# Kernel optimization log

Measured on AMD Instinct MI355X. Metric: run time of the kernel, lower is better.

The kernel has to match this reference:

```python
import jax, jax.numpy as jnp
import numpy as np

BN_EPS = 1e-5


def setup_inputs() -> dict:
    key = jax.random.key(0)
    k1, k2 = jax.random.split(key, 2)
    b, C, h, w = 4, 256, 64, 64
    K = 16  # num_codes is hard-coded to 16 inside __init__
    x = jax.random.normal(k1, (b, C, h, w), dtype=jnp.float32)
    conv_w = jax.random.normal(k2, (K, C), dtype=jnp.float32) * (1.0 / np.sqrt(C))
    bn_gamma = jnp.ones((K,), dtype=jnp.float32)
    bn_beta = jnp.zeros((K,), dtype=jnp.float32)
    return {"x": x, "conv_w": conv_w, "bn_gamma": bn_gamma, "bn_beta": bn_beta}


def reference(x, conv_w, bn_gamma, bn_beta):
    b, C, h, w = x.shape
    K = conv_w.shape[0]
    hw = h * w

    # 1x1 conv (no bias) -> BatchNorm2d (training-mode batch stats) -> ReLU
    cw = jnp.einsum('kc,bchw->bkhw', conv_w, x)          # (b, K, h, w)
    mean = cw.mean(axis=(0, 2, 3))                        # (K,)
    var = cw.var(axis=(0, 2, 3))                          # biased variance, (K,)
    cw = (cw - mean[None, :, None, None]) * jax.lax.rsqrt(var + BN_EPS)[None, :, None, None]
    cw = cw * bn_gamma[None, :, None, None] + bn_beta[None, :, None, None]
    cw = jax.nn.relu(cw)

    cw_flat = cw.reshape(b, K, hw)                        # (b, K, hw)
    scale = cw_flat.mean(axis=2)                          # (b, K)
    # Faithful to torch: flat row-major reinterpretation of (b,K,hw) as (b,hw,K,1)
    r = cw_flat.reshape(b, hw, K, 1)                      # (b, hw, K, 1)

    x2 = x.reshape(b, C, hw).transpose(0, 2, 1)           # (b, hw, C)
    diff = x2[:, :, None, :] - r                          # (b, hw, K, C)

    scaled_l2 = scale[:, :, None] * jnp.sum(diff * diff, axis=1)   # (b, K, C)
    aw = jax.nn.softmax(scaled_l2, axis=1)                # softmax over K, (b, K, C)
    encoded_feat = jnp.sum(aw[:, None, :, :] * diff, axis=1)       # (b, K, C)
    return encoded_feat
```

## Files before the change

kernel.cpp:

```cpp
#include <hip/hip_runtime.h>

#define BN_EPS 1e-5f

#define OFF_PBN     0
#define OFF_PSR     8192
#define OFF_PSX     24576
#define OFF_PSXX    155648
#define OFF_CROSSR  286720
#define OFF_CW      352256
#define OFF_PCX     614400
#define WS_NEED     ((size_t)(OFF_PCX + 2097152) * sizeof(float))

#define CONV_FMA(W, K0)                                  \
    acc[K0][0] = fmaf(W, xv.x, acc[K0][0]);              \
    acc[K0][1] = fmaf(W, xv.y, acc[K0][1]);              \
    acc[K0][2] = fmaf(W, xv.z, acc[K0][2]);              \
    acc[K0][3] = fmaf(W, xv.w, acc[K0][3]);

#define FMA16(v, rp)                                     \
    {                                                    \
        const float4* rq_ = (const float4*)(rp);         \
        float4 r0_ = rq_[0], r1_ = rq_[1];               \
        float4 r2_ = rq_[2], r3_ = rq_[3];               \
        acc[0]  = fmaf(v, r0_.x, acc[0]);                \
        acc[1]  = fmaf(v, r0_.y, acc[1]);                \
        acc[2]  = fmaf(v, r0_.z, acc[2]);                \
        acc[3]  = fmaf(v, r0_.w, acc[3]);                \
        acc[4]  = fmaf(v, r1_.x, acc[4]);                \
        acc[5]  = fmaf(v, r1_.y, acc[5]);                \
        acc[6]  = fmaf(v, r1_.z, acc[6]);                \
        acc[7]  = fmaf(v, r1_.w, acc[7]);                \
        acc[8]  = fmaf(v, r2_.x, acc[8]);                \
        acc[9]  = fmaf(v, r2_.y, acc[9]);                \
        acc[10] = fmaf(v, r2_.z, acc[10]);               \
        acc[11] = fmaf(v, r2_.w, acc[11]);               \
        acc[12] = fmaf(v, r3_.x, acc[12]);               \
        acc[13] = fmaf(v, r3_.y, acc[13]);               \
        acc[14] = fmaf(v, r3_.z, acc[14]);               \
        acc[15] = fmaf(v, r3_.w, acc[15]);               \
    }

__global__ __launch_bounds__(256, 2) void k_conv(const float* __restrict__ x,
                                                 const float* __restrict__ w,
                                                 float* __restrict__ cw,
                                                 float* __restrict__ pbn) {
    __shared__ float wlT[4124];
    __shared__ float bnl[4][32];
    int bid = blockIdx.x;
    int b   = bid >> 6;
    int ich = bid & 63;
    int t   = threadIdx.x;
    int cp  = t & 15;
    int il  = t >> 4;
    int wv  = t >> 6;

    for (int m = t; m < 4096; m += 256) {
        int k = m >> 8, c = m & 255;
        wlT[(c << 4) + ((c >> 5) << 2) + k] = w[m];
    }
    __syncthreads();

    float acc[16][4];
    #pragma unroll
    for (int k = 0; k < 16; ++k) {
        #pragma unroll
        for (int e = 0; e < 4; ++e) acc[k][e] = 0.f;
    }

    const float* xp = x + (size_t)(b * 256 + cp * 16) * 4096 + ich * 64 + il * 4;
    #pragma unroll
    for (int cc = 0; cc < 16; ++cc) {
        float4 xv = *(const float4*)(xp + (size_t)cc * 4096);
        int c = cp * 16 + cc;
        const float4* wr = (const float4*)&wlT[(c << 4) + ((c >> 5) << 2)];
        float4 w0 = wr[0], w1 = wr[1], w2 = wr[2], w3 = wr[3];
        CONV_FMA(w0.x, 0)  CONV_FMA(w0.y, 1)  CONV_FMA(w0.z, 2)  CONV_FMA(w0.w, 3)
        CONV_FMA(w1.x, 4)  CONV_FMA(w1.y, 5)  CONV_FMA(w1.z, 6)  CONV_FMA(w1.w, 7)
        CONV_FMA(w2.x, 8)  CONV_FMA(w2.y, 9)  CONV_FMA(w2.z, 10) CONV_FMA(w2.w, 11)
        CONV_FMA(w3.x, 12) CONV_FMA(w3.y, 13) CONV_FMA(w3.z, 14) CONV_FMA(w3.w, 15)
    }

    float r8[8][4];
    #pragma unroll
    for (int r = 0; r < 8; ++r) {
        #pragma unroll
        for (int e = 0; e < 4; ++e) {
            float lo = acc[r][e]     + __shfl_xor(acc[r][e], 1);
            float hi = acc[r + 8][e] + __shfl_xor(acc[r + 8][e], 1);
            r8[r][e] = (cp & 1) ? hi : lo;
        }
    }
    float r4v[4][4];
    #pragma unroll
    for (int r = 0; r < 4; ++r) {
        #pragma unroll
        for (int e = 0; e < 4; ++e) {
            float lo = r8[r][e]     + __shfl_xor(r8[r][e], 2);
            float hi = r8[r + 4][e] + __shfl_xor(r8[r + 4][e], 2);
            r4v[r][e] = (cp & 2) ? hi : lo;
        }
    }
    float r2[2][4];
    #pragma unroll
    for (int r = 0; r < 2; ++r) {
        #pragma unroll
        for (int e = 0; e < 4; ++e) {
            float lo = r4v[r][e]     + __shfl_xor(r4v[r][e], 4);
            float hi = r4v[r + 2][e] + __shfl_xor(r4v[r + 2][e], 4);
            r2[r][e] = (cp & 4) ? hi : lo;
        }
    }
    float r1[4];
    #pragma unroll
    for (int e = 0; e < 4; ++e) {
        float lo = r2[0][e] + __shfl_xor(r2[0][e], 8);
        float hi = r2[1][e] + __shfl_xor(r2[1][e], 8);
        r1[e] = (cp & 8) ? hi : lo;
    }
    int ko = ((cp & 1) << 3) | (((cp >> 1) & 1) << 2) | (((cp >> 2) & 1) << 1)
           | ((cp >> 3) & 1);

    float4 st;
    st.x = r1[0]; st.y = r1[1]; st.z = r1[2]; st.w = r1[3];
    *(float4*)(cw + (size_t)b * 65536 + (size_t)ko * 4096 + ich * 64 + il * 4) = st;

    float s1 = r1[0] + r1[1] + r1[2] + r1[3];
    float s2 = r1[0]*r1[0] + r1[1]*r1[1] + r1[2]*r1[2] + r1[3]*r1[3];
    #pragma unroll
    for (int m = 16; m <= 32; m <<= 1) {
        s1 += __shfl_xor(s1, m);
        s2 += __shfl_xor(s2, m);
    }
    if ((t & 48) == 0) { bnl[wv][ko] = s1; bnl[wv][16 + ko] = s2; }
    __syncthreads();
    if (t < 32) {
        pbn[bid * 32 + t] = bnl[0][t] + bnl[1][t] + bnl[2][t] + bnl[3][t];
    }
}

template <bool PCX>
__global__ __launch_bounds__(256, 2) void k_main(const float* __restrict__ x,
                                                 const float* __restrict__ gamma,
                                                 const float* __restrict__ beta,
                                                 float* __restrict__ ws,
                                                 float* __restrict__ pcx) {
    __shared__ float xl[8192];
    __shared__ float rl[512];
    __shared__ float red1[256], red2[256];
    __shared__ float bnred[256];
    int bid = blockIdx.x;
    int b   = bid >> 7;
    int s   = bid & 127;
    int kp  = s >> 3;
    int t   = threadIdx.x;

    {
        int col = t & 31, row0 = t >> 5;
        float p = 0.f;
        for (int m = row0; m < 256; m += 8) p += ws[OFF_PBN + m * 32 + col];
        bnred[t] = p;
    }
    __syncthreads();
    float s1 = 0.f, s2 = 0.f;
    #pragma unroll
    for (int j = 0; j < 8; ++j) {
        s1 += bnred[j * 32 + kp];
        s2 += bnred[j * 32 + 16 + kp];
    }
    float mean = s1 * (1.f / 16384.f);
    float var  = s2 * (1.f / 16384.f) - mean * mean;
    float aa   = gamma[kp] * rsqrtf(var + BN_EPS);
    float bb   = beta[kp] - mean * aa;

    #pragma unroll
    for (int j = 0; j < 8; ++j) {
        int F  = j * 256 + t;
        int cc = F >> 3, i4 = F & 7;
        const float* pa = x + (size_t)(b * 256 + cc) * 4096 + s * 32 + i4 * 4;
        float4 v = *(const float4*)pa;
        int ib = i4 * 4;
        xl[(ib + 0) * 256 + (cc ^ (ib + 0))] = v.x;
        xl[(ib + 1) * 256 + (cc ^ (ib + 1))] = v.y;
        xl[(ib + 2) * 256 + (cc ^ (ib + 2))] = v.z;
        xl[(ib + 3) * 256 + (cc ^ (ib + 3))] = v.w;
    }

    const float* cwp = ws + OFF_CW + (size_t)b * 65536 + (size_t)kp * 4096
                     + (size_t)(s & 7) * 512;
    float sr = 0.f, srr = 0.f;
    #pragma unroll
    for (int j = 0; j < 2; ++j) {
        float v = cwp[t + j * 256];
        v = fmaxf(fmaf(v, aa, bb), 0.f);
        rl[t + j * 256] = v;
        sr += v; srr += v * v;
    }
    red1[t] = sr; red2[t] = srr;
    __syncthreads();

    if (t < 16) {
        float a1 = 0.f, a2 = 0.f;
        for (int m = t; m < 256; m += 16) { a1 += red1[m]; a2 += red2[m]; }
        ws[OFF_PSR + bid * 32 + t]      = a1;
        ws[OFF_PSR + bid * 32 + 16 + t] = a2;
    }

    int c = t;
    float acc[16];
    #pragma unroll
    for (int k = 0; k < 16; ++k) acc[k] = 0.f;
    float xs = 0.f, xs2 = 0.f;
    #pragma unroll
    for (int ii = 0; ii < 32; ++ii) {
        float xv = xl[ii * 256 + (c ^ ii)];
        xs += xv; xs2 += xv * xv;
        FMA16(xv, rl + ii * 16);
    }

    ws[OFF_PSX  + bid * 256 + c] = xs;
    ws[OFF_PSXX + bid * 256 + c] = xs2;
    if (PCX) {
        float* pp = pcx + (size_t)(bid * 16) * 256 + c;
        #pragma unroll
        for (int k = 0; k < 16; ++k) pp[(size_t)k * 256] = acc[k];
    } else {
        #pragma unroll
        for (int k = 0; k < 16; ++k)
            atomicAdd(ws + OFF_CROSSR + (b * 16 + k) * 256 + c, acc[k]);
    }
}

__global__ __launch_bounds__(256) void k_red(const float* __restrict__ pcx,
                                             float* __restrict__ crossr) {
    int bid = blockIdx.x;
    int b  = bid >> 6;
    int k  = (bid >> 2) & 15;
    int sg = bid & 3;
    int c  = threadIdx.x;
    float acc = 0.f;
    #pragma unroll 8
    for (int m = 0; m < 32; ++m) {
        int sl = sg * 32 + m;
        acc += pcx[(size_t)((b * 128 + sl) * 16 + k) * 256 + c];
    }
    crossr[((sg * 4 + b) * 16 + k) * 256 + c] = acc;
}

__global__ __launch_bounds__(256) void k_final(const float* __restrict__ ws,
                                               float* __restrict__ out) {
    __shared__ float srl[4096];
    __shared__ float fin[48];
    int b = blockIdx.x;
    int t = threadIdx.x;

    const float* psr = ws + OFF_PSR + (size_t)b * 128 * 32;
    #pragma unroll
    for (int j = 0; j < 16; ++j) srl[j * 256 + t] = psr[j * 256 + t];
    __syncthreads();

    if (t < 16) {
        float v = 0.f;
        for (int s = 0; s < 128; ++s) v += srl[s * 32 + t];
        fin[t] = v;
    } else if (t < 32) {
        int k = t - 16;
        float v = 0.f;
        for (int s = 0; s < 128; ++s) v += srl[s * 32 + 16 + k];
        fin[16 + k] = v;
    } else if (t < 48) {
        int kp = t - 32;
        float v = 0.f;
        for (int s = kp * 8; s < kp * 8 + 8; ++s)
            for (int k2 = 0; k2 < 16; ++k2) v += srl[s * 32 + k2];
        fin[32 + kp] = v;
    }
    __syncthreads();

    int c = t;
    float sx = 0.f, sxx = 0.f;
    const float* psx  = ws + OFF_PSX  + (size_t)b * 128 * 256;
    const float* psxx = ws + OFF_PSXX + (size_t)b * 128 * 256;
    for (int p = 0; p < 128; ++p) {
        sx  += psx[p * 256 + c];
        sxx += psxx[p * 256 + c];
    }

    float sl2[16];
    float mx = -1e30f;
    #pragma unroll
    for (int k = 0; k < 16; ++k) {
        float cr = 0.f;
        #pragma unroll
        for (int sg = 0; sg < 4; ++sg)
            cr += ws[OFF_CROSSR + ((sg * 4 + b) * 16 + k) * 256 + c];
        float v = fin[32 + k] * (1.f / 4096.f) * (sxx - 2.f * cr + fin[16 + k]);
        sl2[k] = v;
        mx = fmaxf(mx, v);
    }
    float den = 0.f;
    #pragma unroll
    for (int k = 0; k < 16; ++k) {
        float e = __expf(sl2[k] - mx);
        sl2[k] = e;
        den += e;
    }
    float inv = 1.f / den;
    #pragma unroll
    for (int k = 0; k < 16; ++k)
        out[(size_t)(b * 16 + k) * 256 + c] = sl2[k] * inv * (sx - fin[k]);
}

extern "C" void kernel_launch(void* const* d_in, const int* in_sizes, int n_in,
                              void* d_out, int out_size, void* d_ws, size_t ws_size,
                              hipStream_t stream) {
    const float* x     = (const float*)d_in[0];
    const float* w     = (const float*)d_in[1];
    const float* gamma = (const float*)d_in[2];
    const float* beta  = (const float*)d_in[3];
    float* ws  = (float*)d_ws;
    float* out = (float*)d_out;

    bool use_pcx = ws_size >= WS_NEED;

    k_conv<<<256, 256, 0, stream>>>(x, w, ws + OFF_CW, ws + OFF_PBN);
    if (use_pcx) {
        k_main<true><<<512, 256, 0, stream>>>(x, gamma, beta, ws, ws + OFF_PCX);
        k_red<<<256, 256, 0, stream>>>(ws + OFF_PCX, ws + OFF_CROSSR);
    } else {
        hipMemsetAsync(ws + OFF_CROSSR, 0, 65536 * sizeof(float), stream);
        k_main<false><<<512, 256, 0, stream>>>(x, gamma, beta, ws, nullptr);
    }
    k_final<<<4, 256, 0, stream>>>(ws, out);
}
```

Before: 102.3 us.

## Restructure conv kernel to stage x tile in LDS across 512 blocks

```diff
diff --git a/kernel.cpp b/kernel.cpp
--- a/kernel.cpp
+++ b/kernel.cpp
@@ -3,19 +3,13 @@
 #define BN_EPS 1e-5f
 
 #define OFF_PBN     0
-#define OFF_PSR     8192
-#define OFF_PSX     24576
-#define OFF_PSXX    155648
-#define OFF_CROSSR  286720
-#define OFF_CW      352256
-#define OFF_PCX     614400
+#define OFF_PSR     16384
+#define OFF_PSX     32768
+#define OFF_PSXX    163840
+#define OFF_CROSSR  294912
+#define OFF_CW      360448
+#define OFF_PCX     622592
 #define WS_NEED     ((size_t)(OFF_PCX + 2097152) * sizeof(float))
-
-#define CONV_FMA(W, K0)                                  \
-    acc[K0][0] = fmaf(W, xv.x, acc[K0][0]);              \
-    acc[K0][1] = fmaf(W, xv.y, acc[K0][1]);              \
-    acc[K0][2] = fmaf(W, xv.z, acc[K0][2]);              \
-    acc[K0][3] = fmaf(W, xv.w, acc[K0][3]);
 
 #define FMA16(v, rp)                                     \
     {                                                    \
@@ -41,104 +35,75 @@
     }
 
 __global__ __launch_bounds__(256, 2) void k_conv(const float* __restrict__ x,
-                                                 const float* __restrict__ w,
+                                                 const float* __restrict__ wq,
                                                  float* __restrict__ cw,
                                                  float* __restrict__ pbn) {
+    __shared__ float xl[10240];
     __shared__ float wlT[4124];
-    __shared__ float bnl[4][32];
+    __shared__ float comb[512];
+    __shared__ float bnr1[128], bnr2[128];
     int bid = blockIdx.x;
-    int b   = bid >> 6;
-    int ich = bid & 63;
+    int b   = bid >> 7;
+    int s   = bid & 127;
     int t   = threadIdx.x;
-    int cp  = t & 15;
-    int il  = t >> 4;
-    int wv  = t >> 6;
+    int k   = t & 15;
+    int q   = t >> 4;
+    int iq  = q & 7;
+    int h   = q >> 3;
 
     for (int m = t; m < 4096; m += 256) {
-        int k = m >> 8, c = m & 255;
-        wlT[(c << 4) + ((c >> 5) << 2) + k] = w[m];
-    }
-    __syncthreads();
-
-    float acc[16][4];
-    #pragma unroll
-    for (int k = 0; k < 16; ++k) {
+        int kk = m >> 8, c = m & 255;
+        wlT[(c << 4) + ((c >> 5) << 2) + kk] = wq[m];
+    }
+    #pragma unroll
+    for (int j = 0; j < 8; ++j) {
+        int F  = j * 256 + t;
+        int cc = F >> 3, i4 = F & 7;
+        float4 v = *(const float4*)(x + (size_t)(b * 256 + cc) * 4096
+                                    + s * 32 + i4 * 4);
+        xl[cc * 40 + i4 * 4 + 0] = v.x;
+        xl[cc * 40 + i4 * 4 + 1] = v.y;
+        xl[cc * 40 + i4 * 4 + 2] = v.z;
+        xl[cc * 40 + i4 * 4 + 3] = v.w;
+    }
+    __syncthreads();
+
+    float a0 = 0.f, a1 = 0.f, a2 = 0.f, a3 = 0.f;
+    int c0 = h * 128;
+    #pragma unroll 8
+    for (int cc = 0; cc < 128; ++cc) {
+        int c = c0 + cc;
+        float4 xv = *(const float4*)&xl[c * 40 + iq * 4];
+        float wv  = wlT[(c << 4) + ((c >> 5) << 2) + k];
+        a0 = fmaf(wv, xv.x, a0);
+        a1 = fmaf(wv, xv.y, a1);
+        a2 = fmaf(wv, xv.z, a2);
+        a3 = fmaf(wv, xv.w, a3);
+    }
+    if (h == 1) {
+        int p = t & 127;
+        comb[p * 4 + 0] = a0; comb[p * 4 + 1] = a1;
+        comb[p * 4 + 2] = a2; comb[p * 4 + 3] = a3;
+    }
+    __syncthreads();
+    if (h == 0) {
+        a0 += comb[t * 4 + 0]; a1 += comb[t * 4 + 1];
+        a2 += comb[t * 4 + 2]; a3 += comb[t * 4 + 3];
+        float4 o; o.x = a0; o.y = a1; o.z = a2; o.w = a3;
+        *(float4*)(cw + (size_t)b * 65536 + (size_t)k * 4096 + s * 32 + iq * 4) = o;
+        bnr1[iq * 16 + k] = a0 + a1 + a2 + a3;
+        bnr2[iq * 16 + k] = a0 * a0 + a1 * a1 + a2 * a2 + a3 * a3;
+    }
+    __syncthreads();
+    if (t < 16) {
+        float s1 = 0.f, s2 = 0.f;
         #pragma unroll
-        for (int e = 0; e < 4; ++e) acc[k][e] = 0.f;
-    }
-
-    const float* xp = x + (size_t)(b * 256 + cp * 16) * 4096 + ich * 64 + il * 4;
-    #pragma unroll
-    for (int cc = 0; cc < 16; ++cc) {
-        float4 xv = *(const float4*)(xp + (size_t)cc * 4096);
-        int c = cp * 16 + cc;
-        const float4* wr = (const float4*)&wlT[(c << 4) + ((c >> 5) << 2)];
-        float4 w0 = wr[0], w1 = wr[1], w2 = wr[2], w3 = wr[3];
-        CONV_FMA(w0.x, 0)  CONV_FMA(w0.y, 1)  CONV_FMA(w0.z, 2)  CONV_FMA(w0.w, 3)
-        CONV_FMA(w1.x, 4)  CONV_FMA(w1.y, 5)  CONV_FMA(w1.z, 6)  CONV_FMA(w1.w, 7)
-        CONV_FMA(w2.x, 8)  CONV_FMA(w2.y, 9)  CONV_FMA(w2.z, 10) CONV_FMA(w2.w, 11)
-        CONV_FMA(w3.x, 12) CONV_FMA(w3.y, 13) CONV_FMA(w3.z, 14) CONV_FMA(w3.w, 15)
-    }
-
-    float r8[8][4];
-    #pragma unroll
-    for (int r = 0; r < 8; ++r) {
-        #pragma unroll
-        for (int e = 0; e < 4; ++e) {
-            float lo = acc[r][e]     + __shfl_xor(acc[r][e], 1);
-            float hi = acc[r + 8][e] + __shfl_xor(acc[r + 8][e], 1);
-            r8[r][e] = (cp & 1) ? hi : lo;
-        }
-    }
-    float r4v[4][4];
-    #pragma unroll
-    for (int r = 0; r < 4; ++r) {
-        #pragma unroll
-        for (int e = 0; e < 4; ++e) {
-            float lo = r8[r][e]     + __shfl_xor(r8[r][e], 2);
-            float hi = r8[r + 4][e] + __shfl_xor(r8[r + 4][e], 2);
-            r4v[r][e] = (cp & 2) ? hi : lo;
-        }
-    }
-    float r2[2][4];
-    #pragma unroll
-    for (int r = 0; r < 2; ++r) {
-        #pragma unroll
-        for (int e = 0; e < 4; ++e) {
-            float lo = r4v[r][e]     + __shfl_xor(r4v[r][e], 4);
-            float hi = r4v[r + 2][e] + __shfl_xor(r4v[r + 2][e], 4);
-            r2[r][e] = (cp & 4) ? hi : lo;
-        }
-    }
-    float r1[4];
-    #pragma unroll
-    for (int e = 0; e < 4; ++e) {
-        float lo = r2[0][e] + __shfl_xor(r2[0][e], 8);
-        float hi = r2[1][e] + __shfl_xor(r2[1][e], 8);
-        r1[e] = (cp & 8) ? hi : lo;
-    }
-    int ko = ((cp & 1) << 3) | (((cp >> 1) & 1) << 2) | (((cp >> 2) & 1) << 1)
-           | ((cp >> 3) & 1);
-
-    float4 st;
-    st.x = r1[0]; st.y = r1[1]; st.z = r1[2]; st.w = r1[3];
-    *(float4*)(cw + (size_t)b * 65536 + (size_t)ko * 4096 + ich * 64 + il * 4) = st;
-
-    float s1 = r1[0] + r1[1] + r1[2] + r1[3];
-    float s2 = r1[0]*r1[0] + r1[1]*r1[1] + r1[2]*r1[2] + r1[3]*r1[3];
-    #pragma unroll
-    for (int m = 16; m <= 32; m <<= 1) {
-        s1 += __shfl_xor(s1, m);
-        s2 += __shfl_xor(s2, m);
-    }
-    if ((t & 48) == 0) { bnl[wv][ko] = s1; bnl[wv][16 + ko] = s2; }
-    __syncthreads();
-    if (t < 32) {
-        pbn[bid * 32 + t] = bnl[0][t] + bnl[1][t] + bnl[2][t] + bnl[3][t];
-    }
-}
-
-template <bool PCX>
+        for (int j = 0; j < 8; ++j) { s1 += bnr1[j * 16 + t]; s2 += bnr2[j * 16 + t]; }
+        pbn[bid * 32 + t]      = s1;
+        pbn[bid * 32 + 16 + t] = s2;
+    }
+}
+
 __global__ __launch_bounds__(256, 2) void k_main(const float* __restrict__ x,
                                                  const float* __restrict__ gamma,
                                                  const float* __restrict__ beta,
@@ -157,7 +122,7 @@
     {
         int col = t & 31, row0 = t >> 5;
         float p = 0.f;
-        for (int m = row0; m < 256; m += 8) p += ws[OFF_PBN + m * 32 + col];
+        for (int m = row0; m < 512; m += 8) p += ws[OFF_PBN + m * 32 + col];
         bnred[t] = p;
     }
     __syncthreads();
@@ -219,15 +184,9 @@
 
     ws[OFF_PSX  + bid * 256 + c] = xs;
     ws[OFF_PSXX + bid * 256 + c] = xs2;
-    if (PCX) {
-        float* pp = pcx + (size_t)(bid * 16) * 256 + c;
-        #pragma unroll
-        for (int k = 0; k < 16; ++k) pp[(size_t)k * 256] = acc[k];
-    } else {
-        #pragma unroll
-        for (int k = 0; k < 16; ++k)
-            atomicAdd(ws + OFF_CROSSR + (b * 16 + k) * 256 + c, acc[k]);
-    }
+    float* pp = pcx + (size_t)(bid * 16) * 256 + c;
+    #pragma unroll
+    for (int k = 0; k < 16; ++k) pp[(size_t)k * 256] = acc[k];
 }
 
 __global__ __launch_bounds__(256) void k_red(const float* __restrict__ pcx,
@@ -320,15 +279,8 @@
     float* ws  = (float*)d_ws;
     float* out = (float*)d_out;
 
-    bool use_pcx = ws_size >= WS_NEED;
-
-    k_conv<<<256, 256, 0, stream>>>(x, w, ws + OFF_CW, ws + OFF_PBN);
-    if (use_pcx) {
-        k_main<true><<<512, 256, 0, stream>>>(x, gamma, beta, ws, ws + OFF_PCX);
-        k_red<<<256, 256, 0, stream>>>(ws + OFF_PCX, ws + OFF_CROSSR);
-    } else {
-        hipMemsetAsync(ws + OFF_CROSSR, 0, 65536 * sizeof(float), stream);
-        k_main<false><<<512, 256, 0, stream>>>(x, gamma, beta, ws, nullptr);
-    }
+    k_conv<<<512, 256, 0, stream>>>(x, w, ws + OFF_CW, ws + OFF_PBN);
+    k_main<<<512, 256, 0, stream>>>(x, gamma, beta, ws, ws + OFF_PCX);
+    k_red<<<256, 256, 0, stream>>>(ws + OFF_PCX, ws + OFF_CROSSR);
     k_final<<<4, 256, 0, stream>>>(ws, out);
 }
```

Measured after the change: 108.3 us. 5.9% more time.
